# Kernel tuning notes

Measured on AMD Instinct MI355X. Metric: run time of the kernel, lower is better.

## Reference

```python
import jax, jax.numpy as jnp
import numpy as np

N_NODES = 100000
N_EDGES = 1600000
IN_CH, MID_CH, BOT_CH = 128, 128, 64


def setup_inputs() -> dict:
    key = jax.random.key(0)
    ks = jax.random.split(key, 10)
    x = jax.random.normal(ks[0], (N_NODES, IN_CH), dtype=jnp.float32)
    edge_index = jax.random.randint(ks[1], (2, N_EDGES), 0, N_NODES, dtype=jnp.int64)
    s = 0.05
    # GCNConv weights follow torch Linear convention: out = x @ W.T + b (bias added post-aggregation)
    W1 = jax.random.normal(ks[2], (MID_CH, IN_CH), dtype=jnp.float32) * s
    b1 = jnp.zeros((MID_CH,), dtype=jnp.float32)
    W2 = jax.random.normal(ks[3], (BOT_CH, MID_CH), dtype=jnp.float32) * s
    b2 = jnp.zeros((BOT_CH,), dtype=jnp.float32)
    W3 = jax.random.normal(ks[4], (MID_CH, BOT_CH), dtype=jnp.float32) * s
    b3 = jnp.zeros((MID_CH,), dtype=jnp.float32)
    W4 = jax.random.normal(ks[5], (IN_CH, MID_CH), dtype=jnp.float32) * s
    b4 = jnp.zeros((IN_CH,), dtype=jnp.float32)
    return {"x": x, "edge_index": edge_index,
            "W1": W1, "b1": b1, "W2": W2, "b2": b2,
            "W3": W3, "b3": b3, "W4": W4, "b4": b4}


def _gcn_conv(x, src, dst, norm, W, b, n):
    # linear transform first (small GEMM), then gather-normalize-scatter
    h = x @ W.T                                   # [N, out]
    msg = h[src] * norm[:, None]                  # [E+N, out] gathered messages
    out = jax.ops.segment_sum(msg, dst, num_segments=n)
    return out + b


def reference(x, edge_index, W1, b1, W2, b2, W3, b3, W4, b4):
    n = N_NODES
    # add self-loops (PyG GCNConv default)
    loop = jnp.arange(n, dtype=edge_index.dtype)
    src = jnp.concatenate([edge_index[0], loop])
    dst = jnp.concatenate([edge_index[1], loop])
    # symmetric degree normalization: deg includes self-loops -> deg >= 1
    deg = jax.ops.segment_sum(jnp.ones_like(dst, dtype=x.dtype), dst, num_segments=n)
    dinv = jax.lax.rsqrt(deg)
    norm = dinv[src] * dinv[dst]                  # [E+N]
    # encoder
    h = jax.nn.relu(_gcn_conv(x, src, dst, norm, W1, b1, n))
    z = _gcn_conv(h, src, dst, norm, W2, b2, n)
    # decoder
    h = jax.nn.relu(_gcn_conv(z, src, dst, norm, W3, b3, n))
    out = _gcn_conv(h, src, dst, norm, W4, b4, n)
    return out
```

## Files before the change

kernel.cpp:

```cpp
#include <hip/hip_runtime.h>

typedef unsigned int u32;
typedef unsigned short u16;
typedef short bf16x4 __attribute__((ext_vector_type(4)));
typedef short bf16x8 __attribute__((ext_vector_type(8)));
typedef float f32x4 __attribute__((ext_vector_type(4)));

__device__ inline u16 f2bf_rne(float f) {
    u32 b = __float_as_uint(f);
    return (u16)((b + 0x7FFFu + ((b >> 16) & 1u)) >> 16);
}
__device__ inline u32 packbf2(float lo, float hi) {
    return (u32)f2bf_rne(lo) | ((u32)f2bf_rne(hi) << 16);
}
__device__ inline float bf2f(u16 h) { return __uint_as_float((u32)h << 16); }
__device__ inline float2 bfpair(u32 q) {
    float2 f;
    f.x = __uint_as_float(q << 16);
    f.y = __uint_as_float(q & 0xFFFF0000u);
    return f;
}

__global__ void k_detect(const int* __restrict__ p, int n_int32, u32* __restrict__ flag) {
    __shared__ int s[256];
    int tid = threadIdx.x;
    int acc = 0;
    int limit = n_int32 < 2048 ? n_int32 : 2048;
    for (int i = 1 + 2 * tid; i < limit; i += 512) acc |= p[i];
    s[tid] = acc;
    __syncthreads();
    for (int o = 128; o > 0; o >>= 1) {
        if (tid < o) s[tid] |= s[tid + o];
        __syncthreads();
    }
    if (tid == 0) *flag = (s[0] == 0) ? 1u : 0u;
}

__global__ void k_convert(const void* __restrict__ p, int n, const u32* __restrict__ flag,
                          int* __restrict__ out) {
    int i = blockIdx.x * blockDim.x + threadIdx.x;
    if (i >= n) return;
    if (*flag) out[i] = (int)((const long long*)p)[i];
    else       out[i] = ((const int*)p)[i];
}

template <int CIN, int COUT>
__global__ void k_wpack(const float* __restrict__ W, u16* __restrict__ Wpk) {
    int i = blockIdx.x * 256 + threadIdx.x;
    if (i >= CIN * COUT) return;
    int o = i / CIN, k = i % CIN;
    int fi = o >> 4, l15 = o & 15;
    int ks = k >> 5, w = k & 31;
    int h = w >> 4, l4 = (w & 15) >> 2, off = w & 3;
    int lane = l4 * 16 + l15;
    int e = h * 4 + off;
    constexpr int KS = CIN / 32;
    Wpk[(size_t)(((fi * KS + ks) * 64 + lane) * 8 + e)] = f2bf_rne(W[i]);
}

__global__ void k_init(u32* __restrict__ deg, u32* __restrict__ cnt, int N) {
    int i = blockIdx.x * blockDim.x + threadIdx.x;
    if (i < N) { deg[i] = 1u; cnt[i] = 0u; }
}

__global__ __launch_bounds__(256) void k_count(const int* __restrict__ dst,
                                               u32* __restrict__ deg, int E, int N) {
    int xcd = blockIdx.x & 7;
    int sub = blockIdx.x >> 3;
    int nsub = gridDim.x >> 3;
    int lo = (int)((long long)N * xcd >> 3);
    int hi = (int)((long long)N * (xcd + 1) >> 3);
    for (int e = sub * 256 + threadIdx.x; e < E; e += nsub * 256) {
        int d = dst[e];
        if (d >= lo && d < hi) atomicAdd(&deg[d], 1u);
    }
}

__global__ void k_dinv(const u32* __restrict__ deg, float* __restrict__ dinv, int N) {
    int i = blockIdx.x * blockDim.x + threadIdx.x;
    if (i < N) dinv[i] = rsqrtf((float)deg[i]);
}

__global__ void k_scan_a(const u32* __restrict__ deg, u32* __restrict__ partial, int N) {
    __shared__ u32 s[256];
    int tid = threadIdx.x;
    int base = blockIdx.x * 1024 + tid * 4;
    u32 sum = 0;
#pragma unroll
    for (int j = 0; j < 4; ++j) {
        int v = base + j;
        sum += (v < N) ? (deg[v] - 1u) : 0u;
    }
    s[tid] = sum;
    __syncthreads();
    for (int o = 128; o > 0; o >>= 1) {
        if (tid < o) s[tid] += s[tid + o];
        __syncthreads();
    }
    if (tid == 0) partial[blockIdx.x] = s[0];
}

__global__ void k_scan_b(u32* __restrict__ partial, int NB, int* __restrict__ row_ptr, int N) {
    __shared__ u32 s[128];
    int tid = threadIdx.x;
    u32 v = (tid < NB) ? partial[tid] : 0u;
    s[tid] = v;
    __syncthreads();
    for (int off = 1; off < 128; off <<= 1) {
        u32 t = (tid >= off) ? s[tid - off] : 0u;
        __syncthreads();
        s[tid] += t;
        __syncthreads();
    }
    if (tid < NB) partial[tid] = s[tid] - v;
    if (tid == 127) row_ptr[N] = (int)s[127];
}

__global__ void k_scan_c(const u32* __restrict__ deg, const u32* __restrict__ partial,
                         int* __restrict__ row_ptr, int N) {
    __shared__ u32 s[256];
    int tid = threadIdx.x;
    int base = blockIdx.x * 1024 + tid * 4;
    u32 vals[4];
    u32 sum = 0;
#pragma unroll
    for (int j = 0; j < 4; ++j) {
        int v = base + j;
        vals[j] = (v < N) ? (deg[v] - 1u) : 0u;
        sum += vals[j];
    }
    s[tid] = sum;
    __syncthreads();
    for (int off = 1; off < 256; off <<= 1) {
        u32 t = (tid >= off) ? s[tid - off] : 0u;
        __syncthreads();
        s[tid] += t;
        __syncthreads();
    }
    u32 run = s[tid] - sum + partial[blockIdx.x];
#pragma unroll
    for (int j = 0; j < 4; ++j) {
        int v = base + j;
        if (v < N) row_ptr[v] = (int)run;
        run += vals[j];
    }
}

__global__ __launch_bounds__(256) void k_fill(const int* __restrict__ src,
                                              const int* __restrict__ dst,
                                              const int* __restrict__ row_ptr,
                                              u32* __restrict__ cnt,
                                              int* __restrict__ col, int E, int N) {
    int xcd = blockIdx.x & 7;
    int sub = blockIdx.x >> 3;
    int nsub = gridDim.x >> 3;
    int lo = (int)((long long)N * xcd >> 3);
    int hi = (int)((long long)N * (xcd + 1) >> 3);
    for (int e = sub * 256 + threadIdx.x; e < E; e += nsub * 256) {
        int d = dst[e];
        if (d >= lo && d < hi) {
            int pos = row_ptr[d] + (int)atomicAdd(&cnt[d], 1u);
            col[pos] = src[e];
        }
    }
}

template <int CIN, int COUT, int MODE, bool IN_F32>
__global__ __launch_bounds__(512, 2) void k_mgemm(const void* __restrict__ Xv,
                                                  const u16* __restrict__ Wpk,
                                                  const float* __restrict__ aux,
                                                  u16* __restrict__ Gout, int N) {
    constexpr int PITCH = CIN + 8;
    constexpr int KS = CIN / 32;
    constexpr int NT = COUT / 32;
    __shared__ __align__(16) u16 sX[64 * PITCH];

    int tid = threadIdx.x, wid = tid >> 6, lane = tid & 63;
    int l15 = lane & 15, l4 = lane >> 4;
    int rg = wid >> 1;
    int cg = wid & 1;
    int rowbase = blockIdx.x * 64;

    bf16x8 wfrag[NT][KS];
#pragma unroll
    for (int nt = 0; nt < NT; ++nt) {
        int fi = cg * NT + nt;
#pragma unroll
        for (int ks = 0; ks < KS; ++ks)
            wfrag[nt][ks] = *(const bf16x8*)&Wpk[(size_t)(((fi * KS + ks) * 64 + lane) * 8)];
    }

    if (IN_F32) {
        const float* Xf = (const float*)Xv;
        for (int i = tid * 8; i < 64 * CIN; i += 512 * 8) {
            int r = i / CIN, k = i % CIN;
            int row = rowbase + r;
            if (row >= N) row = N - 1;
            const float4* xp = (const float4*)(Xf + (size_t)row * CIN + k);
            float4 a = xp[0], b = xp[1];
            uint4 pk;
            pk.x = packbf2(a.x, a.y);
            pk.y = packbf2(a.z, a.w);
            pk.z = packbf2(b.x, b.y);
            pk.w = packbf2(b.z, b.w);
            *(uint4*)&sX[r * PITCH + k] = pk;
        }
    } else {
        const u16* Xb = (const u16*)Xv;
        for (int i = tid * 8; i < 64 * CIN; i += 512 * 8) {
            int r = i / CIN, k = i % CIN;
            int row = rowbase + r;
            if (row >= N) row = N - 1;
            *(bf16x8*)&sX[r * PITCH + k] = *(const bf16x8*)&Xb[(size_t)row * CIN + k];
        }
    }
    __syncthreads();

    f32x4 acc[NT];
#pragma unroll
    for (int nt = 0; nt < NT; ++nt) acc[nt] = (f32x4){0.f, 0.f, 0.f, 0.f};

    const u16* xrow = &sX[(rg * 16 + l15) * PITCH + 4 * l4];

#pragma unroll
    for (int ks = 0; ks < KS; ++ks) {
        bf16x4 a0 = *(const bf16x4*)(xrow + ks * 32);
        bf16x4 a1 = *(const bf16x4*)(xrow + ks * 32 + 16);
        bf16x8 av = __builtin_shufflevector(a0, a1, 0, 1, 2, 3, 4, 5, 6, 7);
#pragma unroll
        for (int nt = 0; nt < NT; ++nt)
            acc[nt] = __builtin_amdgcn_mfma_f32_16x16x32_bf16(av, wfrag[nt][ks], acc[nt], 0, 0, 0);
    }

    float bv[NT];
    if (MODE == 1) {
#pragma unroll
        for (int nt = 0; nt < NT; ++nt) bv[nt] = aux[cg * (COUT / 2) + nt * 16 + l15];
    }
#pragma unroll
    for (int i = 0; i < 4; ++i) {
        int row = rowbase + rg * 16 + 4 * l4 + i;
        if (row < N) {
            float s = (MODE == 0) ? aux[row] : 0.f;
#pragma unroll
            for (int nt = 0; nt < NT; ++nt) {
                float a = acc[nt][i];
                float o = (MODE == 0) ? a * s : fmaxf(a + bv[nt], 0.f);
                Gout[(size_t)row * COUT + cg * (COUT / 2) + nt * 16 + l15] = f2bf_rne(o);
            }
        }
    }
}

template <bool OUT_BF16, bool RELU, bool HAS_BIAS>
__global__ __launch_bounds__(256) void k_spmm128(const u32* __restrict__ Gq,
                                                 const int* __restrict__ rp,
                                                 const int* __restrict__ col,
                                                 const float* __restrict__ dinv,
                                                 const float* __restrict__ bias,
                                                 void* __restrict__ Y, int N) {
    int wid = threadIdx.x >> 6, lane = threadIdx.x & 63;
    int v0 = blockIdx.x * 8 + wid * 2;
    if (v0 >= N) return;
    int v1 = v0 + 1;
    bool has1 = (v1 < N);

    float2 acc0 = bfpair(Gq[(size_t)v0 * 64 + lane]);
    int e0 = rp[v0], f0 = rp[v0 + 1];
    float2 acc1 = {0.f, 0.f};
    int e1 = 0, f1 = 0;
    if (has1) {
        acc1 = bfpair(Gq[(size_t)v1 * 64 + lane]);
        e1 = f0; f1 = rp[v1 + 1];
    }

    while (e0 + 8 <= f0 && e1 + 8 <= f1) {
        int u0[8], u1[8];
#pragma unroll
        for (int j = 0; j < 8; ++j) u0[j] = col[e0 + j];
#pragma unroll
        for (int j = 0; j < 8; ++j) u1[j] = col[e1 + j];
        u32 q0[8], q1[8];
#pragma unroll
        for (int j = 0; j < 8; ++j) q0[j] = Gq[(size_t)u0[j] * 64 + lane];
#pragma unroll
        for (int j = 0; j < 8; ++j) q1[j] = Gq[(size_t)u1[j] * 64 + lane];
#pragma unroll
        for (int j = 0; j < 8; ++j) {
            float2 a = bfpair(q0[j]);
            acc0.x += a.x; acc0.y += a.y;
        }
#pragma unroll
        for (int j = 0; j < 8; ++j) {
            float2 a = bfpair(q1[j]);
            acc1.x += a.x; acc1.y += a.y;
        }
        e0 += 8; e1 += 8;
    }
    for (; e0 + 8 <= f0; e0 += 8) {
        int u[8];
#pragma unroll
        for (int j = 0; j < 8; ++j) u[j] = col[e0 + j];
        u32 q[8];
#pragma unroll
        for (int j = 0; j < 8; ++j) q[j] = Gq[(size_t)u[j] * 64 + lane];
#pragma unroll
        for (int j = 0; j < 8; ++j) {
            float2 a = bfpair(q[j]);
            acc0.x += a.x; acc0.y += a.y;
        }
    }
    for (; e1 + 8 <= f1; e1 += 8) {
        int u[8];
#pragma unroll
        for (int j = 0; j < 8; ++j) u[j] = col[e1 + j];
        u32 q[8];
#pragma unroll
        for (int j = 0; j < 8; ++j) q[j] = Gq[(size_t)u[j] * 64 + lane];
#pragma unroll
        for (int j = 0; j < 8; ++j) {
            float2 a = bfpair(q[j]);
            acc1.x += a.x; acc1.y += a.y;
        }
    }
    for (; e0 < f0; ++e0) {
        float2 a = bfpair(Gq[(size_t)col[e0] * 64 + lane]);
        acc0.x += a.x; acc0.y += a.y;
    }
    for (; e1 < f1; ++e1) {
        float2 a = bfpair(Gq[(size_t)col[e1] * 64 + lane]);
        acc1.x += a.x; acc1.y += a.y;
    }

    {
        float s = dinv[v0];
        float rx = acc0.x * s, ry = acc0.y * s;
        if (HAS_BIAS) { rx += bias[2 * lane]; ry += bias[2 * lane + 1]; }
        if (RELU) { rx = fmaxf(rx, 0.f); ry = fmaxf(ry, 0.f); }
        if (OUT_BF16) ((u32*)Y)[(size_t)v0 * 64 + lane] = packbf2(rx, ry);
        else {
            float2 o2; o2.x = rx; o2.y = ry;
            *(float2*)((float*)Y + (size_t)v0 * 128 + 2 * lane) = o2;
        }
    }
    if (has1) {
        float s = dinv[v1];
        float rx = acc1.x * s, ry = acc1.y * s;
        if (HAS_BIAS) { rx += bias[2 * lane]; ry += bias[2 * lane + 1]; }
        if (RELU) { rx = fmaxf(rx, 0.f); ry = fmaxf(ry, 0.f); }
        if (OUT_BF16) ((u32*)Y)[(size_t)v1 * 64 + lane] = packbf2(rx, ry);
        else {
            float2 o2; o2.x = rx; o2.y = ry;
            *(float2*)((float*)Y + (size_t)v1 * 128 + 2 * lane) = o2;
        }
    }
}

template <bool OUT_BF16, bool RELU, bool HAS_BIAS, bool PRESCALE>
__global__ __launch_bounds__(256) void k_spmm64(const u16* __restrict__ G16,
                                                const int* __restrict__ rp,
                                                const int* __restrict__ col,
                                                const float* __restrict__ dinv,
                                                const float* __restrict__ bias,
                                                void* __restrict__ Y, int N) {
    int wid = threadIdx.x >> 6, lane = threadIdx.x & 63;
    int v0 = blockIdx.x * 8 + wid * 2;
    if (v0 >= N) return;
    int v1 = v0 + 1;
    bool has1 = (v1 < N);

    float acc0 = bf2f(G16[(size_t)v0 * 64 + lane]);
    int e0 = rp[v0], f0 = rp[v0 + 1];
    float acc1 = 0.f;
    int e1 = 0, f1 = 0;
    if (has1) {
        acc1 = bf2f(G16[(size_t)v1 * 64 + lane]);
        e1 = f0; f1 = rp[v1 + 1];
    }

    while (e0 + 8 <= f0 && e1 + 8 <= f1) {
        int u0[8], u1[8];
#pragma unroll
        for (int j = 0; j < 8; ++j) u0[j] = col[e0 + j];
#pragma unroll
        for (int j = 0; j < 8; ++j) u1[j] = col[e1 + j];
        u16 g0[8], g1[8];
#pragma unroll
        for (int j = 0; j < 8; ++j) g0[j] = G16[(size_t)u0[j] * 64 + lane];
#pragma unroll
        for (int j = 0; j < 8; ++j) g1[j] = G16[(size_t)u1[j] * 64 + lane];
        acc0 += ((bf2f(g0[0]) + bf2f(g0[1])) + (bf2f(g0[2]) + bf2f(g0[3]))) +
                ((bf2f(g0[4]) + bf2f(g0[5])) + (bf2f(g0[6]) + bf2f(g0[7])));
        acc1 += ((bf2f(g1[0]) + bf2f(g1[1])) + (bf2f(g1[2]) + bf2f(g1[3]))) +
                ((bf2f(g1[4]) + bf2f(g1[5])) + (bf2f(g1[6]) + bf2f(g1[7])));
        e0 += 8; e1 += 8;
    }
    for (; e0 + 8 <= f0; e0 += 8) {
        int u[8];
#pragma unroll
        for (int j = 0; j < 8; ++j) u[j] = col[e0 + j];
        u16 g[8];
#pragma unroll
        for (int j = 0; j < 8; ++j) g[j] = G16[(size_t)u[j] * 64 + lane];
        acc0 += ((bf2f(g[0]) + bf2f(g[1])) + (bf2f(g[2]) + bf2f(g[3]))) +
                ((bf2f(g[4]) + bf2f(g[5])) + (bf2f(g[6]) + bf2f(g[7])));
    }
    for (; e1 + 8 <= f1; e1 += 8) {
        int u[8];
#pragma unroll
        for (int j = 0; j < 8; ++j) u[j] = col[e1 + j];
        u16 g[8];
#pragma unroll
        for (int j = 0; j < 8; ++j) g[j] = G16[(size_t)u[j] * 64 + lane];
        acc1 += ((bf2f(g[0]) + bf2f(g[1])) + (bf2f(g[2]) + bf2f(g[3]))) +
                ((bf2f(g[4]) + bf2f(g[5])) + (bf2f(g[6]) + bf2f(g[7])));
    }
    for (; e0 < f0; ++e0) acc0 += bf2f(G16[(size_t)col[e0] * 64 + lane]);
    for (; e1 < f1; ++e1) acc1 += bf2f(G16[(size_t)col[e1] * 64 + lane]);

    {
        float s = dinv[v0];
        float r = acc0 * s;
        if (HAS_BIAS) r += bias[lane];
        if (RELU) r = fmaxf(r, 0.f);
        if (PRESCALE) r *= s;
        if (OUT_BF16) ((u16*)Y)[(size_t)v0 * 64 + lane] = f2bf_rne(r);
        else          ((float*)Y)[(size_t)v0 * 64 + lane] = r;
    }
    if (has1) {
        float s = dinv[v1];
        float r = acc1 * s;
        if (HAS_BIAS) r += bias[lane];
        if (RELU) r = fmaxf(r, 0.f);
        if (PRESCALE) r *= s;
        if (OUT_BF16) ((u16*)Y)[(size_t)v1 * 64 + lane] = f2bf_rne(r);
        else          ((float*)Y)[(size_t)v1 * 64 + lane] = r;
    }
}

extern "C" void kernel_launch(void* const* d_in, const int* in_sizes, int n_in,
                              void* d_out, int out_size, void* d_ws, size_t ws_size,
                              hipStream_t stream) {
    const float* x  = (const float*)d_in[0];
    const void*  ei = d_in[1];
    const float* W1 = (const float*)d_in[2];
    const float* b1 = (const float*)d_in[3];
    const float* W2 = (const float*)d_in[4];
    const float* b2 = (const float*)d_in[5];
    const float* W3 = (const float*)d_in[6];
    const float* b3 = (const float*)d_in[7];
    const float* W4 = (const float*)d_in[8];
    const float* b4 = (const float*)d_in[9];

    const int N = in_sizes[0] / 128;
    const int E = in_sizes[1] / 2;

    size_t off = 0;
    auto alloc = [&](size_t bytes) -> void* {
        void* p = (char*)d_ws + off;
        off += (bytes + 255) & ~(size_t)255;
        return p;
    };
    u32*   flag    = (u32*)  alloc(4);
    int*   src32   = (int*)  alloc((size_t)E * 4);
    int*   dst32   = (int*)  alloc((size_t)E * 4);
    u32*   deg     = (u32*)  alloc((size_t)N * 4);
    float* dinv    = (float*)alloc((size_t)N * 4);
    int*   row_ptr = (int*)  alloc((size_t)(N + 1) * 4);
    u32*   cnt     = (u32*)  alloc((size_t)N * 4);
    u32*   partial = (u32*)  alloc(256 * 4);
    int*   col     = (int*)  alloc((size_t)E * 4);
    u16*   Wp1     = (u16*)  alloc(128 * 128 * 2);
    u16*   Wp2     = (u16*)  alloc(64 * 128 * 2);
    u16*   Wp3     = (u16*)  alloc(128 * 64 * 2);
    u16*   Wp4     = (u16*)  alloc(128 * 128 * 2);
    u16*   BUF1    = (u16*)  alloc((size_t)N * 128 * 2);
    u16*   BUF2    = (u16*)  alloc((size_t)N * 128 * 2);
    u16*   BUF3    = (u16*)  alloc((size_t)N * 64 * 2);
    u16*   Zbf     = (u16*)d_out;

    const int n2 = 2 * E;
    const int NB = (N + 1023) / 1024;

    k_detect<<<1, 256, 0, stream>>>((const int*)ei, n2, flag);
    k_convert<<<(n2 + 255) / 256, 256, 0, stream>>>(ei, n2, flag, src32);
    int* dstp = src32 + E;
    k_init<<<(N + 255) / 256, 256, 0, stream>>>(deg, cnt, N);
    k_count<<<1024, 256, 0, stream>>>(dstp, deg, E, N);
    k_dinv<<<(N + 255) / 256, 256, 0, stream>>>(deg, dinv, N);
    k_scan_a<<<NB, 256, 0, stream>>>(deg, partial, N);
    k_scan_b<<<1, 128, 0, stream>>>(partial, NB, row_ptr, N);
    k_scan_c<<<NB, 256, 0, stream>>>(deg, partial, row_ptr, N);
    k_fill<<<1024, 256, 0, stream>>>(src32, dstp, row_ptr, cnt, col, E, N);
    (void)dst32;

    k_wpack<128, 128><<<(128 * 128 + 255) / 256, 256, 0, stream>>>(W1, Wp1);
    k_wpack<128, 64><<<(128 * 64 + 255) / 256, 256, 0, stream>>>(W2, Wp2);
    k_wpack<64, 128><<<(64 * 128 + 255) / 256, 256, 0, stream>>>(W3, Wp3);
    k_wpack<128, 128><<<(128 * 128 + 255) / 256, 256, 0, stream>>>(W4, Wp4);

    const int gM = (N + 63) / 64;
    const int gS = (N + 7) / 8;

    k_mgemm<128, 128, 0, true><<<gM, 512, 0, stream>>>(x, Wp1, dinv, BUF1, N);
    k_spmm128<true, true, true><<<gS, 256, 0, stream>>>((const u32*)BUF1, row_ptr, col, dinv, b1, BUF2, N);

    k_mgemm<128, 64, 0, false><<<gM, 512, 0, stream>>>(BUF2, Wp2, dinv, BUF3, N);
    k_spmm64<true, false, true, true><<<gS, 256, 0, stream>>>(BUF3, row_ptr, col, dinv, b2, Zbf, N);

    k_spmm64<true, false, false, false><<<gS, 256, 0, stream>>>(Zbf, row_ptr, col, dinv, b2, BUF1, N);
    k_mgemm<64, 128, 1, false><<<gM, 512, 0, stream>>>(BUF1, Wp3, b3, BUF2, N);

    k_mgemm<128, 128, 0, false><<<gM, 512, 0, stream>>>(BUF2, Wp4, dinv, BUF1, N);
    k_spmm128<false, false, true><<<gS, 256, 0, stream>>>((const u32*)BUF1, row_ptr, col, dinv, b4, d_out, N);
}
```

Measured before the change: 496.4 us.

## Make GEMM persistent over row tiles and stage epilogue through LDS for coalesced stores

The MFMA GEMM kernel now runs a capped grid of blocks, each looping over several 64-row tiles. Weight fragments are loaded into registers once per block instead of once per tile. Output is staged in a shared-memory tile and written back as 16-byte coalesced chunks rather than scattered 2-byte stores. This adds extra shared memory, an extra barrier per tile and a higher occupancy hint, which may raise register pressure.

New measurement: 490.2 us. About the same (-1.3%).

```diff
diff --git a/kernel.cpp b/kernel.cpp
--- a/kernel.cpp
+++ b/kernel.cpp
@@ -166,20 +166,23 @@
 }
 
 template <int CIN, int COUT, int MODE, bool IN_F32>
-__global__ __launch_bounds__(512, 2) void k_mgemm(const void* __restrict__ Xv,
+__global__ __launch_bounds__(512, 4) void k_mgemm(const void* __restrict__ Xv,
                                                   const u16* __restrict__ Wpk,
                                                   const float* __restrict__ aux,
-                                                  u16* __restrict__ Gout, int N) {
+                                                  u16* __restrict__ Gout, int N,
+                                                  int tiles, int tpb) {
     constexpr int PITCH = CIN + 8;
+    constexpr int EPITCH = COUT + 8;
     constexpr int KS = CIN / 32;
     constexpr int NT = COUT / 32;
+    constexpr int CHUNKS = COUT / 8;
     __shared__ __align__(16) u16 sX[64 * PITCH];
+    __shared__ __align__(16) u16 sE[64 * EPITCH];
 
     int tid = threadIdx.x, wid = tid >> 6, lane = tid & 63;
     int l15 = lane & 15, l4 = lane >> 4;
     int rg = wid >> 1;
     int cg = wid & 1;
-    int rowbase = blockIdx.x * 64;
 
     bf16x8 wfrag[NT][KS];
 #pragma unroll
@@ -189,65 +192,80 @@
         for (int ks = 0; ks < KS; ++ks)
             wfrag[nt][ks] = *(const bf16x8*)&Wpk[(size_t)(((fi * KS + ks) * 64 + lane) * 8)];
     }
-
-    if (IN_F32) {
-        const float* Xf = (const float*)Xv;
-        for (int i = tid * 8; i < 64 * CIN; i += 512 * 8) {
-            int r = i / CIN, k = i % CIN;
-            int row = rowbase + r;
-            if (row >= N) row = N - 1;
-            const float4* xp = (const float4*)(Xf + (size_t)row * CIN + k);
-            float4 a = xp[0], b = xp[1];
-            uint4 pk;
-            pk.x = packbf2(a.x, a.y);
-            pk.y = packbf2(a.z, a.w);
-            pk.z = packbf2(b.x, b.y);
-            pk.w = packbf2(b.z, b.w);
-            *(uint4*)&sX[r * PITCH + k] = pk;
-        }
-    } else {
-        const u16* Xb = (const u16*)Xv;
-        for (int i = tid * 8; i < 64 * CIN; i += 512 * 8) {
-            int r = i / CIN, k = i % CIN;
-            int row = rowbase + r;
-            if (row >= N) row = N - 1;
-            *(bf16x8*)&sX[r * PITCH + k] = *(const bf16x8*)&Xb[(size_t)row * CIN + k];
-        }
-    }
-    __syncthreads();
-
-    f32x4 acc[NT];
-#pragma unroll
-    for (int nt = 0; nt < NT; ++nt) acc[nt] = (f32x4){0.f, 0.f, 0.f, 0.f};
-
-    const u16* xrow = &sX[(rg * 16 + l15) * PITCH + 4 * l4];
-
-#pragma unroll
-    for (int ks = 0; ks < KS; ++ks) {
-        bf16x4 a0 = *(const bf16x4*)(xrow + ks * 32);
-        bf16x4 a1 = *(const bf16x4*)(xrow + ks * 32 + 16);
-        bf16x8 av = __builtin_shufflevector(a0, a1, 0, 1, 2, 3, 4, 5, 6, 7);
-#pragma unroll
-        for (int nt = 0; nt < NT; ++nt)
-            acc[nt] = __builtin_amdgcn_mfma_f32_16x16x32_bf16(av, wfrag[nt][ks], acc[nt], 0, 0, 0);
-    }
-
     float bv[NT];
     if (MODE == 1) {
 #pragma unroll
         for (int nt = 0; nt < NT; ++nt) bv[nt] = aux[cg * (COUT / 2) + nt * 16 + l15];
     }
-#pragma unroll
-    for (int i = 0; i < 4; ++i) {
-        int row = rowbase + rg * 16 + 4 * l4 + i;
-        if (row < N) {
-            float s = (MODE == 0) ? aux[row] : 0.f;
+
+    int t0 = blockIdx.x * tpb;
+    int t1 = t0 + tpb; if (t1 > tiles) t1 = tiles;
+
+    for (int t = t0; t < t1; ++t) {
+        int rowbase = t * 64;
+
+        if (IN_F32) {
+            const float* Xf = (const float*)Xv;
+            for (int i = tid * 8; i < 64 * CIN; i += 512 * 8) {
+                int r = i / CIN, k = i % CIN;
+                int row = rowbase + r;
+                if (row >= N) row = N - 1;
+                const float4* xp = (const float4*)(Xf + (size_t)row * CIN + k);
+                float4 a = xp[0], b = xp[1];
+                uint4 pk;
+                pk.x = packbf2(a.x, a.y);
+                pk.y = packbf2(a.z, a.w);
+                pk.z = packbf2(b.x, b.y);
+                pk.w = packbf2(b.z, b.w);
+                *(uint4*)&sX[r * PITCH + k] = pk;
+            }
+        } else {
+            const u16* Xb = (const u16*)Xv;
+            for (int i = tid * 8; i < 64 * CIN; i += 512 * 8) {
+                int r = i / CIN, k = i % CIN;
+                int row = rowbase + r;
+                if (row >= N) row = N - 1;
+                *(bf16x8*)&sX[r * PITCH + k] = *(const bf16x8*)&Xb[(size_t)row * CIN + k];
+            }
+        }
+        __syncthreads();
+
+        f32x4 acc[NT];
+#pragma unroll
+        for (int nt = 0; nt < NT; ++nt) acc[nt] = (f32x4){0.f, 0.f, 0.f, 0.f};
+
+        const u16* xrow = &sX[(rg * 16 + l15) * PITCH + 4 * l4];
+#pragma unroll
+        for (int ks = 0; ks < KS; ++ks) {
+            bf16x4 a0 = *(const bf16x4*)(xrow + ks * 32);
+            bf16x4 a1 = *(const bf16x4*)(xrow + ks * 32 + 16);
+            bf16x8 av = __builtin_shufflevector(a0, a1, 0, 1, 2, 3, 4, 5, 6, 7);
+#pragma unroll
+            for (int nt = 0; nt < NT; ++nt)
+                acc[nt] = __builtin_amdgcn_mfma_f32_16x16x32_bf16(av, wfrag[nt][ks], acc[nt], 0, 0, 0);
+        }
+
+#pragma unroll
+        for (int i = 0; i < 4; ++i) {
+            int rl = rg * 16 + 4 * l4 + i;
+            int row = rowbase + rl;
+            int rc = row < N ? row : N - 1;
+            float s = (MODE == 0) ? aux[rc] : 0.f;
 #pragma unroll
             for (int nt = 0; nt < NT; ++nt) {
                 float a = acc[nt][i];
                 float o = (MODE == 0) ? a * s : fmaxf(a + bv[nt], 0.f);
-                Gout[(size_t)row * COUT + cg * (COUT / 2) + nt * 16 + l15] = f2bf_rne(o);
+                sE[rl * EPITCH + cg * (COUT / 2) + nt * 16 + l15] = f2bf_rne(o);
             }
+        }
+        __syncthreads();
+
+        for (int a = tid; a < 64 * CHUNKS; a += 512) {
+            int rl = a / CHUNKS, ch = a % CHUNKS;
+            int row = rowbase + rl;
+            if (row < N)
+                *(uint4*)&Gout[(size_t)row * COUT + ch * 8] =
+                    *(const uint4*)&sE[rl * EPITCH + ch * 8];
         }
     }
 }
@@ -499,18 +517,20 @@
     k_wpack<64, 128><<<(64 * 128 + 255) / 256, 256, 0, stream>>>(W3, Wp3);
     k_wpack<128, 128><<<(128 * 128 + 255) / 256, 256, 0, stream>>>(W4, Wp4);
 
-    const int gM = (N + 63) / 64;
+    const int tiles = (N + 63) / 64;
+    const int gM = tiles < 512 ? tiles : 512;
+    const int tpb = (tiles + gM - 1) / gM;
     const int gS = (N + 7) / 8;
 
-    k_mgemm<128, 128, 0, true><<<gM, 512, 0, stream>>>(x, Wp1, dinv, BUF1, N);
+    k_mgemm<128, 128, 0, true><<<gM, 512, 0, stream>>>(x, Wp1, dinv, BUF1, N, tiles, tpb);
     k_spmm128<true, true, true><<<gS, 256, 0, stream>>>((const u32*)BUF1, row_ptr, col, dinv, b1, BUF2, N);
 
-    k_mgemm<128, 64, 0, false><<<gM, 512, 0, stream>>>(BUF2, Wp2, dinv, BUF3, N);
+    k_mgemm<128, 64, 0, false><<<gM, 512, 0, stream>>>(BUF2, Wp2, dinv, BUF3, N, tiles, tpb);
     k_spmm64<true, false, true, true><<<gS, 256, 0, stream>>>(BUF3, row_ptr, col, dinv, b2, Zbf, N);
 
     k_spmm64<true, false, false, false><<<gS, 256, 0, stream>>>(Zbf, row_ptr, col, dinv, b2, BUF1, N);
-    k_mgemm<64, 128, 1, false><<<gM, 512, 0, stream>>>(BUF1, Wp3, b3, BUF2, N);
-
-    k_mgemm<128, 128, 0, false><<<gM, 512, 0, stream>>>(BUF2, Wp4, dinv, BUF1, N);
+    k_mgemm<64, 128, 1, false><<<gM, 512, 0, stream>>>(BUF1, Wp3, b3, BUF2, N, tiles, tpb);
+
+    k_mgemm<128, 128, 0, false><<<gM, 512, 0, stream>>>(BUF2, Wp4, dinv, BUF1, N, tiles, tpb);
     k_spmm128<false, false, true><<<gS, 256, 0, stream>>>((const u32*)BUF1, row_ptr, col, dinv, b4, d_out, N);
 }
```
